# Performance work log

Measured on AMD Instinct MI355X. Metric: run time of the kernel, lower is better.

## Reference

```python
import itertools
import jax, jax.numpy as jnp
import numpy as np

G = 128          # grid points per dimension
D_IN = 3         # domain dimension
D_OUT = 16       # codomain dimension
N_QUERY = 1 << 20


def setup_inputs() -> dict:
    key = jax.random.key(0)
    kx, ky = jax.random.split(key)
    # Sorted, non-uniform grid coordinates in [0, 1] per dimension
    base = jnp.linspace(0.0, 1.0, G, dtype=jnp.float32)
    xs0 = base
    xs1 = base ** 1.5            # non-uniform spacing, still sorted
    xs2 = jnp.sqrt(base)         # non-uniform spacing, still sorted
    # Vector-valued samples on the tensor grid
    y = jax.random.normal(ky, (G, G, G, D_OUT), dtype=jnp.float32)
    # Query points, slightly outside [0,1] to exercise clamped extension
    x = jax.random.uniform(kx, (N_QUERY, D_IN), dtype=jnp.float32,
                           minval=-0.1, maxval=1.1)
    return {"x": x, "y": y, "xs0": xs0, "xs1": xs1, "xs2": xs2}


def _interp_linear_clamped(x, y, xs):
    """Multilinear interpolation of grid function y (G,...,G,D) at x (N,d_in),
    clamped extension. Faithful to _grid_interpolate(method='linear',
    extend='clamped')."""
    d_in = len(xs)
    x_min = jnp.stack([g[0] for g in xs])   # (d_in,)
    x_max = jnp.stack([g[-1] for g in xs])  # (d_in,)
    xq = jnp.clip(x, x_min[None], x_max[None])  # clamp to domain

    left, ts = [], []
    for i, g in enumerate(xs):
        n = g.shape[0]
        # index of left grid point: searchsorted right, minus 1
        li = jnp.searchsorted(g, xq[:, i], side="right") - 1
        # points exactly at the upper boundary belong to the last cell
        li = jnp.where(xq[:, i] == g[-1], li - 1, li)
        li = jnp.clip(li, 0, n - 2)  # after clamping all queries are internal
        t = (xq[:, i] - g[li]) / (g[li + 1] - g[li])  # fractional coordinate
        left.append(li)
        ts.append(t)

    # Accumulate over the 2^d_in cell corners
    result = jnp.zeros((x.shape[0], y.shape[-1]), dtype=y.dtype)
    for exponent in itertools.product((0, 1), repeat=d_in):
        c = jnp.ones_like(ts[0])
        for i in range(d_in):
            c = c * (ts[i] if exponent[i] else 1.0 - ts[i])
        idx = tuple(left[i] + exponent[i] for i in range(d_in))
        val = y[idx]  # (N, D_OUT) gather of corner values
        result = result + c[:, None] * val
    return result


def reference(x, y, xs0, xs1, xs2):
    return _interp_linear_clamped(x, y, [xs0, xs1, xs2])
```

## Files before the change

kernel.cpp:

```cpp
#include <hip/hip_runtime.h>

#define G 128
#define D_OUT 16

__global__ __launch_bounds__(256) void interp3d_kernel(
    const float* __restrict__ x,
    const float* __restrict__ y,
    const float* __restrict__ xs0,
    const float* __restrict__ xs1,
    const float* __restrict__ xs2,
    float* __restrict__ out,
    int nquery)
{
    __shared__ float sxs[3][G];
    const int tid = threadIdx.x;

    for (int i = tid; i < 3 * G; i += 256) {
        float v;
        if (i < G)            v = xs0[i];
        else if (i < 2 * G)   v = xs1[i - G];
        else                  v = xs2[i - 2 * G];
        (&sxs[0][0])[i] = v;
    }
    __syncthreads();

    const int q  = blockIdx.x * 64 + (tid >> 2);
    if (q >= nquery) return;
    const int cg = (tid & 3) * 4;

    int   li[3];
    float t[3];
    #pragma unroll
    for (int d = 0; d < 3; ++d) {
        const float* g = sxs[d];
        float v = x[q * 3 + d];
        v = fminf(fmaxf(v, g[0]), g[G - 1]);
        int idx = 0;
        #pragma unroll
        for (int s = 64; s >= 1; s >>= 1) {
            int cand = idx + s;
            if (g[cand] <= v) idx = cand;
        }
        if (idx > G - 2) idx = G - 2;
        float g0 = g[idx], g1 = g[idx + 1];
        li[d] = idx;
        t[d]  = (v - g0) / (g1 - g0);
    }

    const float w0[3] = { 1.f - t[0], 1.f - t[1], 1.f - t[2] };
    const float w1[3] = { t[0], t[1], t[2] };

    float4 acc = make_float4(0.f, 0.f, 0.f, 0.f);
    #pragma unroll
    for (int e = 0; e < 8; ++e) {
        const int e0 = (e >> 2) & 1, e1 = (e >> 1) & 1, e2 = e & 1;
        const float w = (e0 ? w1[0] : w0[0]) * (e1 ? w1[1] : w0[1]) * (e2 ? w1[2] : w0[2]);
        const int idx = ((li[0] + e0) * G + (li[1] + e1)) * G + (li[2] + e2);
        const float4 v = *(const float4*)(y + (size_t)idx * D_OUT + cg);
        acc.x += w * v.x;
        acc.y += w * v.y;
        acc.z += w * v.z;
        acc.w += w * v.w;
    }

    *(float4*)(out + (size_t)q * D_OUT + cg) = acc;
}

extern "C" void kernel_launch(void* const* d_in, const int* in_sizes, int n_in,
                              void* d_out, int out_size, void* d_ws, size_t ws_size,
                              hipStream_t stream) {
    const float* x   = (const float*)d_in[0];
    const float* y   = (const float*)d_in[1];
    const float* xs0 = (const float*)d_in[2];
    const float* xs1 = (const float*)d_in[3];
    const float* xs2 = (const float*)d_in[4];
    float* out = (float*)d_out;

    const int nquery = in_sizes[0] / 3;
    const int blocks = (nquery + 63) / 64;

    hipLaunchKernelGGL(interp3d_kernel, dim3(blocks), dim3(256), 0, stream,
                       x, y, xs0, xs1, xs2, out, nquery);
}
```

Baseline: 108.9 us.

## Bin queries by spatial cell via counting sort before interpolation gathers

Adds a histogram, scan and scatter pipeline that groups queries into 16^3 spatial bins by their grid cell, then runs interpolation over the binned payload with an XCD-aware block remap. The aim is better cache locality for the random 8-corner gathers from the 128 MB grid. The cost is three extra passes with binary searches, global atomics, a single-block scan and a 16 MB payload write and read, plus scattered output writes.

```diff
diff --git a/kernel.cpp b/kernel.cpp
--- a/kernel.cpp
+++ b/kernel.cpp
@@ -2,50 +2,139 @@
 
 #define G 128
 #define D_OUT 16
-
-__global__ __launch_bounds__(256) void interp3d_kernel(
-    const float* __restrict__ x,
-    const float* __restrict__ y,
-    const float* __restrict__ xs0,
-    const float* __restrict__ xs1,
-    const float* __restrict__ xs2,
-    float* __restrict__ out,
-    int nquery)
-{
-    __shared__ float sxs[3][G];
-    const int tid = threadIdx.x;
-
-    for (int i = tid; i < 3 * G; i += 256) {
+#define BIN_SHIFT 3
+#define NBINS (16 * 16 * 16)
+
+
+__device__ __forceinline__ void stage_grids(const float* __restrict__ xs0,
+                                            const float* __restrict__ xs1,
+                                            const float* __restrict__ xs2,
+                                            float (*sxs)[G], int tid, int nthreads)
+{
+    for (int i = tid; i < 3 * G; i += nthreads) {
         float v;
         if (i < G)            v = xs0[i];
         else if (i < 2 * G)   v = xs1[i - G];
         else                  v = xs2[i - 2 * G];
         (&sxs[0][0])[i] = v;
     }
-    __syncthreads();
-
-    const int q  = blockIdx.x * 64 + (tid >> 2);
-    if (q >= nquery) return;
-    const int cg = (tid & 3) * 4;
+}
+
+__device__ __forceinline__ void search1(const float* __restrict__ g, float v,
+                                        int& li, float& t)
+{
+    v = fminf(fmaxf(v, g[0]), g[G - 1]);
+    int idx = 0;
+    #pragma unroll
+    for (int s = 64; s >= 1; s >>= 1) {
+        int cand = idx + s;
+        if (g[cand] <= v) idx = cand;
+    }
+    if (idx > G - 2) idx = G - 2;
+    li = idx;
+    t  = (v - g[idx]) / (g[idx + 1] - g[idx]);
+}
+
+__device__ __forceinline__ int bin_of(int li0, int li1, int li2)
+{
+    return ((li0 >> BIN_SHIFT) << 8) | ((li1 >> BIN_SHIFT) << 4) | (li2 >> BIN_SHIFT);
+}
+
+
+__global__ __launch_bounds__(256) void hist_kernel(
+    const float* __restrict__ x,
+    const float* __restrict__ xs0, const float* __restrict__ xs1, const float* __restrict__ xs2,
+    unsigned int* __restrict__ counts, int n)
+{
+    __shared__ float sxs[3][G];
+    stage_grids(xs0, xs1, xs2, sxs, threadIdx.x, 256);
+    __syncthreads();
+
+    int q = blockIdx.x * 256 + threadIdx.x;
+    if (q >= n) return;
+    int li[3]; float t;
+    #pragma unroll
+    for (int d = 0; d < 3; ++d) search1(sxs[d], x[q * 3 + d], li[d], t);
+    atomicAdd(&counts[bin_of(li[0], li[1], li[2])], 1u);
+}
+
+
+__global__ __launch_bounds__(1024) void scan_kernel(
+    const unsigned int* __restrict__ counts, unsigned int* __restrict__ offsets)
+{
+    __shared__ unsigned int sd[1024];
+    const int t = threadIdx.x;
+    uint4 c = ((const uint4*)counts)[t];
+    unsigned int s = c.x + c.y + c.z + c.w;
+    sd[t] = s;
+    __syncthreads();
+    for (int off = 1; off < 1024; off <<= 1) {
+        unsigned int v = sd[t];
+        unsigned int add = (t >= off) ? sd[t - off] : 0u;
+        __syncthreads();
+        sd[t] = v + add;
+        __syncthreads();
+    }
+    unsigned int excl = sd[t] - s;
+    uint4 o;
+    o.x = excl;
+    o.y = o.x + c.x;
+    o.z = o.y + c.y;
+    o.w = o.z + c.z;
+    ((uint4*)offsets)[t] = o;
+}
+
+
+__global__ __launch_bounds__(256) void scatter_kernel(
+    const float* __restrict__ x,
+    const float* __restrict__ xs0, const float* __restrict__ xs1, const float* __restrict__ xs2,
+    unsigned int* __restrict__ offsets, float4* __restrict__ payload, int n)
+{
+    __shared__ float sxs[3][G];
+    stage_grids(xs0, xs1, xs2, sxs, threadIdx.x, 256);
+    __syncthreads();
+
+    int q = blockIdx.x * 256 + threadIdx.x;
+    if (q >= n) return;
+    float v0 = x[q * 3 + 0], v1 = x[q * 3 + 1], v2 = x[q * 3 + 2];
+    int li[3]; float t;
+    search1(sxs[0], v0, li[0], t);
+    search1(sxs[1], v1, li[1], t);
+    search1(sxs[2], v2, li[2], t);
+    unsigned int slot = atomicAdd(&offsets[bin_of(li[0], li[1], li[2])], 1u);
+    payload[slot] = make_float4(v0, v1, v2, __uint_as_float((unsigned int)q));
+}
+
+
+__global__ __launch_bounds__(256) void interp_sorted_kernel(
+    const float4* __restrict__ payload,
+    const float* __restrict__ y,
+    const float* __restrict__ xs0, const float* __restrict__ xs1, const float* __restrict__ xs2,
+    float* __restrict__ out, int n)
+{
+    __shared__ float sxs[3][G];
+    stage_grids(xs0, xs1, xs2, sxs, threadIdx.x, 256);
+    __syncthreads();
+
+    int bid = blockIdx.x;
+    int nb  = gridDim.x;
+    if ((nb & 7) == 0) {
+        int chunk = nb >> 3;
+        bid = (bid & 7) * chunk + (bid >> 3);
+    }
+
+    const int i = bid * 64 + (threadIdx.x >> 2);
+    if (i >= n) return;
+    const int cg = (threadIdx.x & 3) * 4;
+
+    const float4 p = payload[i];
+    const unsigned int q = __float_as_uint(p.w);
 
     int   li[3];
     float t[3];
-    #pragma unroll
-    for (int d = 0; d < 3; ++d) {
-        const float* g = sxs[d];
-        float v = x[q * 3 + d];
-        v = fminf(fmaxf(v, g[0]), g[G - 1]);
-        int idx = 0;
-        #pragma unroll
-        for (int s = 64; s >= 1; s >>= 1) {
-            int cand = idx + s;
-            if (g[cand] <= v) idx = cand;
-        }
-        if (idx > G - 2) idx = G - 2;
-        float g0 = g[idx], g1 = g[idx + 1];
-        li[d] = idx;
-        t[d]  = (v - g0) / (g1 - g0);
-    }
+    search1(sxs[0], p.x, li[0], t[0]);
+    search1(sxs[1], p.y, li[1], t[1]);
+    search1(sxs[2], p.z, li[2], t[2]);
 
     const float w0[3] = { 1.f - t[0], 1.f - t[1], 1.f - t[2] };
     const float w1[3] = { t[0], t[1], t[2] };
@@ -66,6 +155,39 @@
     *(float4*)(out + (size_t)q * D_OUT + cg) = acc;
 }
 
+
+__global__ __launch_bounds__(256) void interp3d_kernel(
+    const float* __restrict__ x, const float* __restrict__ y,
+    const float* __restrict__ xs0, const float* __restrict__ xs1, const float* __restrict__ xs2,
+    float* __restrict__ out, int nquery)
+{
+    __shared__ float sxs[3][G];
+    stage_grids(xs0, xs1, xs2, sxs, threadIdx.x, 256);
+    __syncthreads();
+
+    const int q = blockIdx.x * 64 + (threadIdx.x >> 2);
+    if (q >= nquery) return;
+    const int cg = (threadIdx.x & 3) * 4;
+
+    int li[3]; float t[3];
+    #pragma unroll
+    for (int d = 0; d < 3; ++d) search1(sxs[d], x[q * 3 + d], li[d], t[d]);
+
+    const float w0[3] = { 1.f - t[0], 1.f - t[1], 1.f - t[2] };
+    const float w1[3] = { t[0], t[1], t[2] };
+
+    float4 acc = make_float4(0.f, 0.f, 0.f, 0.f);
+    #pragma unroll
+    for (int e = 0; e < 8; ++e) {
+        const int e0 = (e >> 2) & 1, e1 = (e >> 1) & 1, e2 = e & 1;
+        const float w = (e0 ? w1[0] : w0[0]) * (e1 ? w1[1] : w0[1]) * (e2 ? w1[2] : w0[2]);
+        const int idx = ((li[0] + e0) * G + (li[1] + e1)) * G + (li[2] + e2);
+        const float4 v = *(const float4*)(y + (size_t)idx * D_OUT + cg);
+        acc.x += w * v.x; acc.y += w * v.y; acc.z += w * v.z; acc.w += w * v.w;
+    }
+    *(float4*)(out + (size_t)q * D_OUT + cg) = acc;
+}
+
 extern "C" void kernel_launch(void* const* d_in, const int* in_sizes, int n_in,
                               void* d_out, int out_size, void* d_ws, size_t ws_size,
                               hipStream_t stream) {
@@ -77,8 +199,31 @@
     float* out = (float*)d_out;
 
     const int nquery = in_sizes[0] / 3;
-    const int blocks = (nquery + 63) / 64;
-
-    hipLaunchKernelGGL(interp3d_kernel, dim3(blocks), dim3(256), 0, stream,
-                       x, y, xs0, xs1, xs2, out, nquery);
-}
+
+    const size_t need = (size_t)2 * NBINS * sizeof(unsigned int)
+                      + (size_t)nquery * sizeof(float4);
+    if (ws_size < need) {
+        const int blocks = (nquery + 63) / 64;
+        hipLaunchKernelGGL(interp3d_kernel, dim3(blocks), dim3(256), 0, stream,
+                           x, y, xs0, xs1, xs2, out, nquery);
+        return;
+    }
+
+    unsigned int* counts  = (unsigned int*)d_ws;
+    unsigned int* offsets = counts + NBINS;
+    float4*       payload = (float4*)(offsets + NBINS);
+
+    hipMemsetAsync(counts, 0, NBINS * sizeof(unsigned int), stream);
+
+    const int b256 = (nquery + 255) / 256;
+    hipLaunchKernelGGL(hist_kernel, dim3(b256), dim3(256), 0, stream,
+                       x, xs0, xs1, xs2, counts, nquery);
+    hipLaunchKernelGGL(scan_kernel, dim3(1), dim3(1024), 0, stream,
+                       counts, offsets);
+    hipLaunchKernelGGL(scatter_kernel, dim3(b256), dim3(256), 0, stream,
+                       x, xs0, xs1, xs2, offsets, payload, nquery);
+
+    const int b64 = (nquery + 63) / 64;
+    hipLaunchKernelGGL(interp_sorted_kernel, dim3(b64), dim3(256), 0, stream,
+                       payload, y, xs0, xs1, xs2, out, nquery);
+}
```

Measured after the change: 434.2 us. 3.99x slower.
